# Performance work log

Measured on AMD Instinct MI355X. Metric: run time of the kernel, lower is better.

## Reference

```python
import jax, jax.numpy as jnp
import numpy as np

COMMIT_LAMBDA = 0.25


def setup_inputs() -> dict:
    key = jax.random.key(0)
    k1, k2 = jax.random.split(key)
    B, C, T = 8, 256, 1024
    NCB, K, D = 2, 8192, 128
    x = jax.random.normal(k1, (B, C, T), dtype=jnp.float32)
    # EMA codebook weights buffer (init: randn * 0.1)
    codebooks = jax.random.normal(k2, (NCB, K, D), dtype=jnp.float32) * 0.1
    return {"x": x, "codebooks": codebooks}


def reference(x, codebooks):
    B, C, T = x.shape
    ncb, K, d = codebooks.shape
    # [B, C, T] -> [B*T, ncb, d]
    xs = x.reshape(B, ncb, d, T).transpose(0, 3, 1, 2).reshape(B * T, ncb, d)
    # squared euclidean distances (argmin-equivalent to cdist)
    x2 = jnp.sum(xs * xs, axis=-1)[..., None]            # [N, ncb, 1]
    c2 = jnp.sum(codebooks * codebooks, axis=-1)[None]    # [1, ncb, K]
    xc = jnp.einsum('bnd,nkd->bnk', xs, codebooks)        # [N, ncb, K]
    d2 = x2 - 2.0 * xc + c2
    idx = jnp.argmin(d2, axis=-1)                         # [N, ncb] int
    # gather nearest code vectors: [N, ncb, d]
    q = codebooks[jnp.arange(ncb)[None, :], idx]
    # straight-through estimator
    q_st = xs + jax.lax.stop_gradient(q - xs)
    # commitment loss (training mode): sum over codebooks of mse(x_i, q_i.detach())
    loss = COMMIT_LAMBDA * jnp.sum(
        jnp.mean((xs - jax.lax.stop_gradient(q)) ** 2, axis=(0, 2))
    )
    # reassemble to [B, C, T]
    quantized = q_st.reshape(B, T, ncb, d).transpose(0, 2, 3, 1).reshape(B, C, T)
    indices = idx.reshape(B, T, ncb).transpose(0, 2, 1)   # [B, ncb, T]
    return quantized, indices, loss
```

## Files before the change

### kernel.cpp

```cpp
#include <hip/hip_runtime.h>
#include <hip/hip_bf16.h>

#define BB   8
#define TT   1024
#define NCBN 2
#define DD   128
#define KK   8192
#define MM   8192

constexpr int OUT_IDX_OFF  = BB * 256 * TT;
constexpr int OUT_LOSS_OFF = OUT_IDX_OFF + BB * NCBN * TT;

#define THR   0.45f
#define QCAP  2048

typedef __attribute__((ext_vector_type(8))) short   short8;
typedef __attribute__((ext_vector_type(4))) float   float4v;

__device__ __forceinline__ unsigned short f2bf(float v) {
    unsigned u = __float_as_uint(v);
    return (unsigned short)((u + 0x7FFFu + ((u >> 16) & 1u)) >> 16);
}

__device__ __forceinline__ unsigned short f2bf_dn(float v) {
    unsigned u = __float_as_uint(v);
    unsigned short h = (unsigned short)(u >> 16);
    if ((u & 0x80000000u) && (u & 0xFFFFu)) ++h;
    return h;
}

__device__ __forceinline__ void gl_lds16(const void* g, void* l) {
    __builtin_amdgcn_global_load_lds(
        (const __attribute__((address_space(1))) unsigned int*)g,
        (__attribute__((address_space(3))) unsigned int*)l, 16, 0, 0);
}

__global__ __launch_bounds__(256)
void pack_x_kernel(const float* __restrict__ x, unsigned short* __restrict__ xbf,
                   float* __restrict__ x2, unsigned long long* __restrict__ pmin) {
    __shared__ float Ld[DD][65];
    const int b = blockIdx.x >> 1, n = blockIdx.x & 1;
    const int t0 = blockIdx.y * 64;
    const int tid = threadIdx.x;

    const float* base = x + ((size_t)(b * 256 + n * 128)) * TT + t0;
    const int dro = tid >> 2, q4 = tid & 3;
#pragma unroll
    for (int half = 0; half < 2; ++half) {
        int d = dro + half * 64;
        const float* rp = base + (size_t)d * TT + q4 * 16;
#pragma unroll
        for (int j = 0; j < 4; ++j) {
            float4 v = *(const float4*)(rp + j * 4);
            int t = q4 * 16 + j * 4;
            Ld[d][t + 0] = v.x; Ld[d][t + 1] = v.y;
            Ld[d][t + 2] = v.z; Ld[d][t + 3] = v.w;
        }
    }
    __syncthreads();

    if (tid < 64) {
        float s = 0.f;
        for (int d = 0; d < DD; ++d) { float v = Ld[d][tid]; s = fmaf(v, v, s); }
        x2[(size_t)n * MM + b * TT + t0 + tid] = s;
        pmin[(size_t)n * MM + b * TT + t0 + tid] = 0xFFFFFFFFFFFFFFFFull;
    }

    unsigned short* orow0 = xbf + ((size_t)n * MM + b * TT + t0) * DD;
#pragma unroll
    for (int pp = 0; pp < 4; ++pp) {
        int u = tid + pp * 256;
        int tt = u >> 4, sg = u & 15;
        unsigned short tmp[8];
#pragma unroll
        for (int j = 0; j < 8; ++j) tmp[j] = f2bf(Ld[sg * 8 + j][tt]);
        uint4 pk;
        pk.x = (unsigned)tmp[0] | ((unsigned)tmp[1] << 16);
        pk.y = (unsigned)tmp[2] | ((unsigned)tmp[3] << 16);
        pk.z = (unsigned)tmp[4] | ((unsigned)tmp[5] << 16);
        pk.w = (unsigned)tmp[6] | ((unsigned)tmp[7] << 16);
        *(uint4*)(orow0 + (size_t)tt * DD + sg * 8) = pk;
    }
}

__global__ __launch_bounds__(256)
void pack_c_kernel(const float* __restrict__ cb, unsigned short* __restrict__ cbf,
                   float* __restrict__ c2, float* __restrict__ out) {
    int g = blockIdx.x * 256 + threadIdx.x;
    if (g == 0) out[OUT_LOSS_OFF] = 0.f;
    const float4* crow = (const float4*)(cb + (size_t)g * DD);
    unsigned short* orow = cbf + (size_t)g * DD;
    float s = 0.f;
#pragma unroll 4
    for (int i2 = 0; i2 < 16; ++i2) {
        float4 v0 = crow[2 * i2];
        float4 v1 = crow[2 * i2 + 1];
        s = fmaf(v0.x, v0.x, s); s = fmaf(v0.y, v0.y, s);
        s = fmaf(v0.z, v0.z, s); s = fmaf(v0.w, v0.w, s);
        s = fmaf(v1.x, v1.x, s); s = fmaf(v1.y, v1.y, s);
        s = fmaf(v1.z, v1.z, s); s = fmaf(v1.w, v1.w, s);
        uint4 pk;
        pk.x = (unsigned)f2bf(v0.x) | ((unsigned)f2bf(v0.y) << 16);
        pk.y = (unsigned)f2bf(v0.z) | ((unsigned)f2bf(v0.w) << 16);
        pk.z = (unsigned)f2bf(v1.x) | ((unsigned)f2bf(v1.y) << 16);
        pk.w = (unsigned)f2bf(v1.z) | ((unsigned)f2bf(v1.w) << 16);
        *(uint4*)(orow + i2 * 8) = pk;
    }
    c2[g] = s;
}

__device__ void rescore_one(int n, int m, int k,
                            const float* __restrict__ x, const float* __restrict__ cb,
                            const float* __restrict__ x2, const float* __restrict__ c2,
                            unsigned long long* __restrict__ pmin) {
    int b = m >> 10, t = m & (TT - 1);
    const float* xp = x + ((size_t)(b * 256 + n * 128)) * TT + t;
    const float* cp = cb + ((size_t)(n * KK + k)) * DD;
    float xc = 0.f;
    for (int d = 0; d < DD; ++d)
        xc = fmaf(xp[(size_t)d * TT], cp[d], xc);
    float u = x2[n * MM + m] - 2.0f * xc;
    float s = u + c2[n * KK + k];
    unsigned long long pk = ((unsigned long long)__float_as_uint(s) << 32) | (unsigned)k;
    atomicMin(pmin + (size_t)n * MM + m, pk);
}

__global__ __launch_bounds__(256, 2)
void screen_kernel(const unsigned short* __restrict__ xbf,
                   const unsigned short* __restrict__ cbf,
                   const float* __restrict__ c2,
                   const float* __restrict__ x,
                   const float* __restrict__ cb32,
                   const float* __restrict__ x2,
                   unsigned long long* __restrict__ pmin) {
    __shared__ __align__(16) unsigned short Csh[2][128 * 128];
    __shared__ float          c2s[2][128];
    __shared__ unsigned int   minU[128];
    __shared__ unsigned int   qcnt;
    __shared__ unsigned int   queue[QCAP];
    __shared__ unsigned short queueY[QCAP];

    const int tid = threadIdx.x;
    const int id  = blockIdx.x;
    const int n   = id & 1;
    const int ks  = (id >> 1) & 3;
    const int qt  = id >> 3;
    const int m0  = qt * 128;
    const int k0  = ks * 2048;

    const int wave = tid >> 6, lane = tid & 63;
    const int cw = wave & 1, qw = wave >> 1;
    const int quad = lane >> 4, l15 = lane & 15;

    int goff[8];
#pragma unroll
    for (int p = 0; p < 8; ++p) {
        int u   = (p * 4 + wave) * 64 + lane;
        int row = u >> 4;
        int seg = (u & 15) ^ (row & 15);
        goff[p] = (row * DD + seg * 8) * 2;
    }

    const char*  asrc0 = (const char*)(cbf + ((size_t)n * KK + k0) * DD);
    const float* c2p   = c2 + (size_t)n * KK + k0;

    {
        const char* qsrc = (const char*)(xbf + ((size_t)n * MM + m0) * DD);
#pragma unroll
        for (int p = 0; p < 8; ++p)
            gl_lds16(qsrc + goff[p], &Csh[0][(p * 4 + wave) * 512]);
#pragma unroll
        for (int p = 0; p < 8; ++p)
            gl_lds16(asrc0 + goff[p], &Csh[1][(p * 4 + wave) * 512]);
    }
    if (tid < 32)  *(float4*)&c2s[1][tid * 4] = *(const float4*)(c2p + tid * 4);
    if (tid < 128) minU[tid] = 0xFFFFFFFFu;
    if (tid == 0)  qcnt = 0;
    __syncthreads();

    short8 bfr[4][4];
#pragma unroll
    for (int tq = 0; tq < 4; ++tq) {
        int q = qw * 64 + tq * 16 + l15;
#pragma unroll
        for (int k4 = 0; k4 < 4; ++k4) {
            int seg = k4 * 4 + quad;
            bfr[tq][k4] = *(const short8*)(&Csh[0][q * 128 + ((seg ^ l15) * 8)]);
        }
    }
    __syncthreads();

    float thr[4] = {3.4e38f, 3.4e38f, 3.4e38f, 3.4e38f};

    for (int it = 0; it <= 16; ++it) {
        const int sb   = it & 1;
        const int cbuf = sb ^ 1;
        const int dcur = (it < 16) ? it : 0;

        if (it < 16) {
            const int dn = (it + 1 < 16) ? (it + 1) : 0;
            const char* src = asrc0 + (size_t)dn * (128 * DD * 2);
#pragma unroll
            for (int p = 0; p < 8; ++p)
                gl_lds16(src + goff[p], &Csh[sb][(p * 4 + wave) * 512]);
            if (tid < 32)
                *(float4*)&c2s[sb][tid * 4] =
                    *(const float4*)(c2p + dn * 128 + tid * 4);
        }

        float4v acc[4][4];
#pragma unroll
        for (int tc = 0; tc < 4; ++tc)
#pragma unroll
            for (int tq = 0; tq < 4; ++tq)
                acc[tc][tq] = (float4v){0.f, 0.f, 0.f, 0.f};

#pragma unroll
        for (int k4 = 0; k4 < 4; ++k4) {
            short8 a[4];
#pragma unroll
            for (int tc = 0; tc < 4; ++tc) {
                int r = cw * 64 + tc * 16 + l15;
                int seg = k4 * 4 + quad;
                a[tc] = *(const short8*)(&Csh[cbuf][r * 128 + ((seg ^ l15) * 8)]);
            }
#pragma unroll
            for (int tc = 0; tc < 4; ++tc)
#pragma unroll
                for (int tq = 0; tq < 4; ++tq)
                    acc[tc][tq] = __builtin_amdgcn_mfma_f32_16x16x32_bf16(
                        a[tc], bfr[tq][k4], acc[tc][tq], 0, 0, 0);
        }

        float cmin[4] = {3.4e38f, 3.4e38f, 3.4e38f, 3.4e38f};
#pragma unroll
        for (int tc = 0; tc < 4; ++tc) {
            float4v c2r = *(const float4v*)(&c2s[cbuf][cw * 64 + tc * 16 + quad * 4]);
#pragma unroll
            for (int tq = 0; tq < 4; ++tq) {
                float y0 = fmaf(-2.0f, acc[tc][tq][0], c2r[0]);
                float y1 = fmaf(-2.0f, acc[tc][tq][1], c2r[1]);
                float y2 = fmaf(-2.0f, acc[tc][tq][2], c2r[2]);
                float y3 = fmaf(-2.0f, acc[tc][tq][3], c2r[3]);
                acc[tc][tq] = (float4v){y0, y1, y2, y3};
                cmin[tq] = fminf(cmin[tq],
                                 fminf(fminf(y0, y1), fminf(y2, y3)));
            }
        }
#pragma unroll
        for (int tq = 0; tq < 4; ++tq) {
            float v = cmin[tq];
            v = fminf(v, __shfl_xor(v, 16, 64));
            v = fminf(v, __shfl_xor(v, 32, 64));
            cmin[tq] = v;
        }

        if (it > 0) {
            float te[4];
#pragma unroll
            for (int tq = 0; tq < 4; ++tq)
                te[tq] = fminf(thr[tq], cmin[tq] + THR);
#pragma unroll
            for (int tc = 0; tc < 4; ++tc) {
#pragma unroll
                for (int tq = 0; tq < 4; ++tq) {
                    float4v yv = acc[tc][tq];
                    float m4 = fminf(fminf(yv[0], yv[1]), fminf(yv[2], yv[3]));
                    if (m4 <= te[tq]) {
#pragma unroll
                        for (int rg = 0; rg < 4; ++rg) {
                            if (yv[rg] <= te[tq]) {
                                unsigned idx  = atomicAdd(&qcnt, 1u);
                                unsigned code = (unsigned)(dcur * 128 + cw * 64 + tc * 16 + quad * 4 + rg);
                                unsigned q    = (unsigned)(qw * 64 + tq * 16 + l15);
                                if (idx < QCAP) {
                                    queue[idx]  = (q << 11) | code;
                                    queueY[idx] = f2bf_dn(yv[rg]);
                                } else {
                                    rescore_one(n, m0 + (int)q, k0 + (int)code,
                                                x, cb32, x2, c2, pmin);
                                }
                            }
                        }
                    }
                }
            }
        }

#pragma unroll
        for (int tq = 0; tq < 4; ++tq) {
            if (quad == 0) {
                unsigned u  = __float_as_uint(cmin[tq]);
                unsigned mu = (u & 0x80000000u) ? ~u : (u | 0x80000000u);
                atomicMin(&minU[qw * 64 + tq * 16 + l15], mu);
            }
        }
        __syncthreads();
        if (it < 16) {
#pragma unroll
            for (int tq = 0; tq < 4; ++tq) {
                unsigned mu = minU[qw * 64 + tq * 16 + l15];
                unsigned u  = (mu & 0x80000000u) ? (mu & 0x7FFFFFFFu) : ~mu;
                thr[tq] = __uint_as_float(u) + THR;
            }
        }
    }

    unsigned total = qcnt; if (total > QCAP) total = QCAP;
    for (unsigned i = tid; i < total; i += 256) {
        unsigned ent = queue[i];
        unsigned q   = ent >> 11;
        unsigned mu  = minU[q];
        unsigned u   = (mu & 0x80000000u) ? (mu & 0x7FFFFFFFu) : ~mu;
        float thrF   = __uint_as_float(u) + THR;
        float yv     = __uint_as_float((unsigned)queueY[i] << 16);
        if (yv <= thrF)
            rescore_one(n, m0 + (int)q, k0 + (int)(ent & 2047u),
                        x, cb32, x2, c2, pmin);
    }
}

__global__ __launch_bounds__(256)
void gather_kernel(const float* __restrict__ x, const float* __restrict__ cb,
                   const unsigned long long* __restrict__ pmin,
                   float* __restrict__ out) {
    __shared__ float Cr[64][DD + 1];
    __shared__ int   kid[64];
    const int b = blockIdx.x >> 1, n = blockIdx.x & 1;
    const int t0 = blockIdx.y * 64;
    const int tid = threadIdx.x;

    if (tid < 64) {
        int t = t0 + tid;
        int k = (int)(pmin[(size_t)n * MM + b * TT + t] & 0xFFFFFFFFull);
        kid[tid] = k;
        out[OUT_IDX_OFF + (b * NCBN + n) * TT + t] = (float)k;
    }
    __syncthreads();

    {
        int row = tid >> 2, q4 = tid & 3;
        const float* cp = cb + ((size_t)n * KK + kid[row]) * DD + q4 * 32;
#pragma unroll
        for (int j = 0; j < 8; ++j) {
            float4 v = *(const float4*)(cp + j * 4);
            int d = q4 * 32 + j * 4;
            Cr[row][d + 0] = v.x; Cr[row][d + 1] = v.y;
            Cr[row][d + 2] = v.z; Cr[row][d + 3] = v.w;
        }
    }
    __syncthreads();

    float lsum = 0.f;
    const float* xb = x  + ((size_t)(b * 256 + n * 128)) * TT + t0;
    float*       ob = out + ((size_t)(b * 256 + n * 128)) * TT + t0;
#pragma unroll
    for (int pp = 0; pp < 8; ++pp) {
        int u  = tid + pp * 256;
        int d  = u >> 4, ts = (u & 15) * 4;
        float4 xv = *(const float4*)(xb + (size_t)d * TT + ts);
        float4 qv = { Cr[ts + 0][d], Cr[ts + 1][d], Cr[ts + 2][d], Cr[ts + 3][d] };
        *(float4*)(ob + (size_t)d * TT + ts) = qv;
        float e;
        e = xv.x - qv.x; lsum = fmaf(e, e, lsum);
        e = xv.y - qv.y; lsum = fmaf(e, e, lsum);
        e = xv.z - qv.z; lsum = fmaf(e, e, lsum);
        e = xv.w - qv.w; lsum = fmaf(e, e, lsum);
    }

#pragma unroll
    for (int o = 32; o > 0; o >>= 1) lsum += __shfl_down(lsum, o, 64);
    __shared__ float wsum[4];
    int lane = tid & 63, w = tid >> 6;
    if (lane == 0) wsum[w] = lsum;
    __syncthreads();
    if (tid == 0) {
        float tot = wsum[0] + wsum[1] + wsum[2] + wsum[3];
        atomicAdd(out + OUT_LOSS_OFF, tot * 2.384185791015625e-7f);
    }
}

extern "C" void kernel_launch(void* const* d_in, const int* in_sizes, int n_in,
                              void* d_out, int out_size, void* d_ws, size_t ws_size,
                              hipStream_t stream) {
    (void)in_sizes; (void)n_in; (void)out_size; (void)ws_size;
    const float* x  = (const float*)d_in[0];
    const float* cb = (const float*)d_in[1];
    float* out = (float*)d_out;

    char* ws = (char*)d_ws;
    unsigned short* xbf = (unsigned short*)(ws);
    unsigned short* cbf = (unsigned short*)(ws + (4u << 20));
    float* x2 = (float*)(ws + (8u << 20));
    float* c2 = (float*)(ws + (8u << 20) + (64u << 10));
    unsigned long long* pmin =
        (unsigned long long*)(ws + (8u << 20) + (128u << 10));

    pack_x_kernel<<<dim3(16, 16), 256, 0, stream>>>(x, xbf, x2, pmin);
    pack_c_kernel<<<dim3(64), 256, 0, stream>>>(cb, cbf, c2, out);

    screen_kernel<<<dim3(512), 256, 0, stream>>>(xbf, cbf, c2, x, cb, x2, pmin);
    gather_kernel<<<dim3(16, 16), 256, 0, stream>>>(x, cb, pmin, out);
}
```

Before: 196.9 us.

## Use 512-thread screen blocks with halved per-wave query tiles and inline candidate filtering

The screening kernel now launches 8 waves per block instead of 4. Each wave covers 32 query rows instead of 64, which halves the accumulator and B-fragment registers and allows higher occupancy. Candidate enqueueing is folded into the distance epilogue and compares against the previous iteration's shared threshold, dropping the current-tile per-wave min tightening. This removes a separate pass, but the looser filter can enqueue more candidates, causing more queue overflow and fp32 rescoring. Each code tile read from LDS is now shared by twice as many waves, which raises LDS read traffic per MFMA.

```diff
diff --git a/kernel.cpp b/kernel.cpp
--- a/kernel.cpp
+++ b/kernel.cpp
@@ -125,7 +125,7 @@
     atomicMin(pmin + (size_t)n * MM + m, pk);
 }
 
-__global__ __launch_bounds__(256, 2)
+__global__ __launch_bounds__(512, 4)
 void screen_kernel(const unsigned short* __restrict__ xbf,
                    const unsigned short* __restrict__ cbf,
                    const float* __restrict__ c2,
@@ -152,10 +152,10 @@
     const int cw = wave & 1, qw = wave >> 1;
     const int quad = lane >> 4, l15 = lane & 15;
 
-    int goff[8];
-#pragma unroll
-    for (int p = 0; p < 8; ++p) {
-        int u   = (p * 4 + wave) * 64 + lane;
+    int goff[4];
+#pragma unroll
+    for (int p = 0; p < 4; ++p) {
+        int u   = (p * 8 + wave) * 64 + lane;
         int row = u >> 4;
         int seg = (u & 15) ^ (row & 15);
         goff[p] = (row * DD + seg * 8) * 2;
@@ -167,21 +167,21 @@
     {
         const char* qsrc = (const char*)(xbf + ((size_t)n * MM + m0) * DD);
 #pragma unroll
-        for (int p = 0; p < 8; ++p)
-            gl_lds16(qsrc + goff[p], &Csh[0][(p * 4 + wave) * 512]);
-#pragma unroll
-        for (int p = 0; p < 8; ++p)
-            gl_lds16(asrc0 + goff[p], &Csh[1][(p * 4 + wave) * 512]);
+        for (int p = 0; p < 4; ++p)
+            gl_lds16(qsrc + goff[p], &Csh[0][(p * 8 + wave) * 512]);
+#pragma unroll
+        for (int p = 0; p < 4; ++p)
+            gl_lds16(asrc0 + goff[p], &Csh[1][(p * 8 + wave) * 512]);
     }
     if (tid < 32)  *(float4*)&c2s[1][tid * 4] = *(const float4*)(c2p + tid * 4);
     if (tid < 128) minU[tid] = 0xFFFFFFFFu;
     if (tid == 0)  qcnt = 0;
     __syncthreads();
 
-    short8 bfr[4][4];
-#pragma unroll
-    for (int tq = 0; tq < 4; ++tq) {
-        int q = qw * 64 + tq * 16 + l15;
+    short8 bfr[2][4];
+#pragma unroll
+    for (int tq = 0; tq < 2; ++tq) {
+        int q = qw * 32 + tq * 16 + l15;
 #pragma unroll
         for (int k4 = 0; k4 < 4; ++k4) {
             int seg = k4 * 4 + quad;
@@ -190,7 +190,7 @@
     }
     __syncthreads();
 
-    float thr[4] = {3.4e38f, 3.4e38f, 3.4e38f, 3.4e38f};
+    float thr[2] = {3.4e38f, 3.4e38f};
 
     for (int it = 0; it <= 16; ++it) {
         const int sb   = it & 1;
@@ -201,18 +201,18 @@
             const int dn = (it + 1 < 16) ? (it + 1) : 0;
             const char* src = asrc0 + (size_t)dn * (128 * DD * 2);
 #pragma unroll
-            for (int p = 0; p < 8; ++p)
-                gl_lds16(src + goff[p], &Csh[sb][(p * 4 + wave) * 512]);
+            for (int p = 0; p < 4; ++p)
+                gl_lds16(src + goff[p], &Csh[sb][(p * 8 + wave) * 512]);
             if (tid < 32)
                 *(float4*)&c2s[sb][tid * 4] =
                     *(const float4*)(c2p + dn * 128 + tid * 4);
         }
 
-        float4v acc[4][4];
+        float4v acc[4][2];
 #pragma unroll
         for (int tc = 0; tc < 4; ++tc)
 #pragma unroll
-            for (int tq = 0; tq < 4; ++tq)
+            for (int tq = 0; tq < 2; ++tq)
                 acc[tc][tq] = (float4v){0.f, 0.f, 0.f, 0.f};
 
 #pragma unroll
@@ -227,59 +227,38 @@
 #pragma unroll
             for (int tc = 0; tc < 4; ++tc)
 #pragma unroll
-                for (int tq = 0; tq < 4; ++tq)
+                for (int tq = 0; tq < 2; ++tq)
                     acc[tc][tq] = __builtin_amdgcn_mfma_f32_16x16x32_bf16(
                         a[tc], bfr[tq][k4], acc[tc][tq], 0, 0, 0);
         }
 
-        float cmin[4] = {3.4e38f, 3.4e38f, 3.4e38f, 3.4e38f};
+        float cmin[2] = {3.4e38f, 3.4e38f};
+        const bool enq = (it > 0);
 #pragma unroll
         for (int tc = 0; tc < 4; ++tc) {
             float4v c2r = *(const float4v*)(&c2s[cbuf][cw * 64 + tc * 16 + quad * 4]);
 #pragma unroll
-            for (int tq = 0; tq < 4; ++tq) {
+            for (int tq = 0; tq < 2; ++tq) {
                 float y0 = fmaf(-2.0f, acc[tc][tq][0], c2r[0]);
                 float y1 = fmaf(-2.0f, acc[tc][tq][1], c2r[1]);
                 float y2 = fmaf(-2.0f, acc[tc][tq][2], c2r[2]);
                 float y3 = fmaf(-2.0f, acc[tc][tq][3], c2r[3]);
-                acc[tc][tq] = (float4v){y0, y1, y2, y3};
-                cmin[tq] = fminf(cmin[tq],
-                                 fminf(fminf(y0, y1), fminf(y2, y3)));
-            }
-        }
-#pragma unroll
-        for (int tq = 0; tq < 4; ++tq) {
-            float v = cmin[tq];
-            v = fminf(v, __shfl_xor(v, 16, 64));
-            v = fminf(v, __shfl_xor(v, 32, 64));
-            cmin[tq] = v;
-        }
-
-        if (it > 0) {
-            float te[4];
-#pragma unroll
-            for (int tq = 0; tq < 4; ++tq)
-                te[tq] = fminf(thr[tq], cmin[tq] + THR);
-#pragma unroll
-            for (int tc = 0; tc < 4; ++tc) {
-#pragma unroll
-                for (int tq = 0; tq < 4; ++tq) {
-                    float4v yv = acc[tc][tq];
-                    float m4 = fminf(fminf(yv[0], yv[1]), fminf(yv[2], yv[3]));
-                    if (m4 <= te[tq]) {
-#pragma unroll
-                        for (int rg = 0; rg < 4; ++rg) {
-                            if (yv[rg] <= te[tq]) {
-                                unsigned idx  = atomicAdd(&qcnt, 1u);
-                                unsigned code = (unsigned)(dcur * 128 + cw * 64 + tc * 16 + quad * 4 + rg);
-                                unsigned q    = (unsigned)(qw * 64 + tq * 16 + l15);
-                                if (idx < QCAP) {
-                                    queue[idx]  = (q << 11) | code;
-                                    queueY[idx] = f2bf_dn(yv[rg]);
-                                } else {
-                                    rescore_one(n, m0 + (int)q, k0 + (int)code,
-                                                x, cb32, x2, c2, pmin);
-                                }
+                float m4 = fminf(fminf(y0, y1), fminf(y2, y3));
+                cmin[tq] = fminf(cmin[tq], m4);
+                if (enq && m4 <= thr[tq]) {
+                    float yv[4] = {y0, y1, y2, y3};
+#pragma unroll
+                    for (int rg = 0; rg < 4; ++rg) {
+                        if (yv[rg] <= thr[tq]) {
+                            unsigned idx  = atomicAdd(&qcnt, 1u);
+                            unsigned code = (unsigned)(dcur * 128 + cw * 64 + tc * 16 + quad * 4 + rg);
+                            unsigned q    = (unsigned)(qw * 32 + tq * 16 + l15);
+                            if (idx < QCAP) {
+                                queue[idx]  = (q << 11) | code;
+                                queueY[idx] = f2bf_dn(yv[rg]);
+                            } else {
+                                rescore_one(n, m0 + (int)q, k0 + (int)code,
+                                            x, cb32, x2, c2, pmin);
                             }
                         }
                     }
@@ -287,19 +266,24 @@
             }
         }
 
-#pragma unroll
-        for (int tq = 0; tq < 4; ++tq) {
-            if (quad == 0) {
-                unsigned u  = __float_as_uint(cmin[tq]);
-                unsigned mu = (u & 0x80000000u) ? ~u : (u | 0x80000000u);
-                atomicMin(&minU[qw * 64 + tq * 16 + l15], mu);
+        if (it < 16) {
+#pragma unroll
+            for (int tq = 0; tq < 2; ++tq) {
+                float v = cmin[tq];
+                v = fminf(v, __shfl_xor(v, 16, 64));
+                v = fminf(v, __shfl_xor(v, 32, 64));
+                if (quad == 0) {
+                    unsigned u  = __float_as_uint(v);
+                    unsigned mu = (u & 0x80000000u) ? ~u : (u | 0x80000000u);
+                    atomicMin(&minU[qw * 32 + tq * 16 + l15], mu);
+                }
             }
         }
         __syncthreads();
         if (it < 16) {
 #pragma unroll
-            for (int tq = 0; tq < 4; ++tq) {
-                unsigned mu = minU[qw * 64 + tq * 16 + l15];
+            for (int tq = 0; tq < 2; ++tq) {
+                unsigned mu = minU[qw * 32 + tq * 16 + l15];
                 unsigned u  = (mu & 0x80000000u) ? (mu & 0x7FFFFFFFu) : ~mu;
                 thr[tq] = __uint_as_float(u) + THR;
             }
@@ -307,7 +291,7 @@
     }
 
     unsigned total = qcnt; if (total > QCAP) total = QCAP;
-    for (unsigned i = tid; i < total; i += 256) {
+    for (unsigned i = tid; i < total; i += 512) {
         unsigned ent = queue[i];
         unsigned q   = ent >> 11;
         unsigned mu  = minU[q];
@@ -399,6 +383,6 @@
     pack_x_kernel<<<dim3(16, 16), 256, 0, stream>>>(x, xbf, x2, pmin);
     pack_c_kernel<<<dim3(64), 256, 0, stream>>>(cb, cbf, c2, out);
 
-    screen_kernel<<<dim3(512), 256, 0, stream>>>(xbf, cbf, c2, x, cb, x2, pmin);
+    screen_kernel<<<dim3(512), 512, 0, stream>>>(xbf, cbf, c2, x, cb, x2, pmin);
     gather_kernel<<<dim3(16, 16), 256, 0, stream>>>(x, cb, pmin, out);
 }
```

Measured after the change: 191.0 us. 3.0% less time.
